# Kernel optimization log

Hardware: AMD Instinct MI355X
Metric: run time of the kernel (lower is better)

The kernel has to match this reference:

```python
import jax, jax.numpy as jnp
import numpy as np
from jax import lax

N, CI, CO, H, W = 2, 256, 256, 64, 64
K, G, DIL, PAD, STRIDE = 3, 8, 1, 1, 1
P = K * K
CG = CO // G  # group channels = 32


def setup_inputs() -> dict:
    key = jax.random.key(0)
    ks = jax.random.split(key, 24)
    r = lambda i, shape, s=1.0: jax.random.normal(ks[i], shape, jnp.float32) * s
    u = lambda i, shape: jax.random.uniform(ks[i], shape, jnp.float32, 0.5, 1.5)
    return dict(
        x=r(0, (N, CI, H, W)),
        conv1_w=r(1, (CO, CI), CI ** -0.5),
        bn1_g=u(2, (CO,)), bn1_b=r(3, (CO,), 0.1), bn1_m=r(4, (CO,), 0.1), bn1_v=u(5, (CO,)),
        inproj_w=r(6, (CO, CO), CO ** -0.5), inproj_b=r(7, (CO,), 0.02),
        dw_w=r(8, (CO, 1, K, K), 0.2), dw_b=r(9, (CO,), 0.02),
        ln_g=u(10, (CO,)), ln_b=r(11, (CO,), 0.02),
        off_w=r(12, (CO, G * P * 2), CO ** -0.5), off_b=jnp.zeros((G * P * 2,), jnp.float32),
        mask_w=r(13, (CO, G * P), CO ** -0.5), mask_b=jnp.zeros((G * P,), jnp.float32),
        outproj_w=r(14, (CO, CO), CO ** -0.5), outproj_b=r(15, (CO,), 0.02),
        bn2_g=u(16, (CO,)), bn2_b=r(17, (CO,), 0.1), bn2_m=r(18, (CO,), 0.1), bn2_v=u(19, (CO,)),
    )


def _bn(x, g, b, m, v, eps):
    # inference-mode BatchNorm2d on NCHW
    return (x - m[:, None, None]) * (g[:, None, None] * lax.rsqrt(v[:, None, None] + eps)) + b[:, None, None]


def _dcn_core(t, offset, mask):
    # t: (N,H,W,C) projected input; offset: (N,H,W,G*P*2); mask: (N,H,W,G,P) softmaxed
    xp = jnp.pad(t, ((0, 0), (PAD, PAD), (PAD, PAD), (0, 0)))
    H_, W_ = H + 2 * PAD, W + 2 * PAD
    # reference points (sample centers), normalized to padded size
    ry = ((DIL * (K - 1)) / 2 + 0.5 + STRIDE * jnp.arange(H, dtype=t.dtype)) / H_
    rx = ((DIL * (K - 1)) / 2 + 0.5 + STRIDE * jnp.arange(W, dtype=t.dtype)) / W_
    base = (DIL * (K - 1)) // 2
    gx = jnp.linspace(-base, -base + (K - 1) * DIL, K, dtype=t.dtype) / W_
    gy = jnp.linspace(-base, -base + (K - 1) * DIL, K, dtype=t.dtype) / H_
    gxx, gyy = jnp.meshgrid(gx, gy, indexing='ij')  # x varies along axis 0 (torch meshgrid order)
    grid = jnp.stack([gxx, gyy], -1).reshape(P, 2)  # (P,2)
    off = offset.reshape(N, H, W, G, P, 2) / jnp.array([W_, H_], t.dtype)
    loc_x = rx[None, None, :, None, None] + grid[:, 0][None, None, None, None] + off[..., 0]  # (N,H,W,G,P)
    loc_y = ry[None, :, None, None, None] + grid[:, 1][None, None, None, None] + off[..., 1]
    # grid_sample(align_corners=False): pixel = norm*size - 0.5
    px = jnp.transpose(loc_x * W_ - 0.5, (0, 3, 1, 2, 4)).reshape(N, G, H * W * P)
    py = jnp.transpose(loc_y * H_ - 0.5, (0, 3, 1, 2, 4)).reshape(N, G, H * W * P)
    # grouped channels-last image: (N,G,H_*W_,CG)
    xg = jnp.transpose(xp.reshape(N, H_, W_, G, CG), (0, 3, 1, 2, 4)).reshape(N, G, H_ * W_, CG)
    x0 = jnp.floor(px)
    y0 = jnp.floor(py)
    wx1 = px - x0
    wy1 = py - y0
    x0i = x0.astype(jnp.int32)
    y0i = y0.astype(jnp.int32)

    def corner(xi, yi, w):
        valid = (xi >= 0) & (xi <= W_ - 1) & (yi >= 0) & (yi <= H_ - 1)
        idx = jnp.clip(yi, 0, H_ - 1) * W_ + jnp.clip(xi, 0, W_ - 1)
        v = jnp.take_along_axis(xg, idx[..., None], axis=2)  # (N,G,M,CG)
        return v * jnp.where(valid, w, 0.0)[..., None]

    sampled = (corner(x0i, y0i, (1 - wx1) * (1 - wy1))
               + corner(x0i + 1, y0i, wx1 * (1 - wy1))
               + corner(x0i, y0i + 1, (1 - wx1) * wy1)
               + corner(x0i + 1, y0i + 1, wx1 * wy1))
    sampled = sampled.reshape(N, G, H * W, P, CG)
    mg = jnp.transpose(mask, (0, 3, 1, 2, 4)).reshape(N, G, H * W, P)
    out = jnp.einsum('nglpc,nglp->nglc', sampled, mg)
    return jnp.transpose(out, (0, 2, 1, 3)).reshape(N, H, W, G * CG)


def reference(x, conv1_w, bn1_g, bn1_b, bn1_m, bn1_v, inproj_w, inproj_b, dw_w, dw_b,
              ln_g, ln_b, off_w, off_b, mask_w, mask_b, outproj_w, outproj_b,
              bn2_g, bn2_b, bn2_m, bn2_v):
    # Conv(inc, ouc, k=1): 1x1 conv (no bias) + BN(eps=1e-3) + SiLU
    y = jnp.einsum('nchw,oc->nohw', x, conv1_w)
    y = jax.nn.silu(_bn(y, bn1_g, bn1_b, bn1_m, bn1_v, 1e-3))
    t = jnp.transpose(y, (0, 2, 3, 1))  # NHWC
    xproj = t @ inproj_w + inproj_b     # input_proj Linear
    # offset/mask branch: depthwise conv (k=3,s=1,p=1) -> LN over C -> GELU
    z = lax.conv_general_dilated(y, dw_w, (1, 1), ((PAD, PAD), (PAD, PAD)),
                                 feature_group_count=CO,
                                 dimension_numbers=('NCHW', 'OIHW', 'NCHW')) + dw_b[None, :, None, None]
    z = jnp.transpose(z, (0, 2, 3, 1))
    mu = jnp.mean(z, -1, keepdims=True)
    var = jnp.var(z, -1, keepdims=True)
    z = (z - mu) * lax.rsqrt(var + 1e-5) * ln_g + ln_b
    z = jax.nn.gelu(z, approximate=False)
    offset = z @ off_w + off_b  # (N,H,W,G*P*2)
    mask = jax.nn.softmax((z @ mask_w + mask_b).reshape(N, H, W, G, P), axis=-1)
    s = _dcn_core(xproj, offset, mask)
    s = s @ outproj_w + outproj_b  # output_proj Linear
    o = jnp.transpose(s, (0, 3, 1, 2))  # back to NCHW
    return jax.nn.silu(_bn(o, bn2_g, bn2_b, bn2_m, bn2_v, 1e-5))
```

## Files before the change

### kernel.cpp

```cpp
#include <hip/hip_runtime.h>
#include <hip/hip_fp16.h>
#include <math.h>

#define CC    256
#define HH    64
#define WW    64
#define HWSZ  4096
#define NPIX  8192
#define MT    32
#define TT    16
#define ASTR  264

typedef __attribute__((ext_vector_type(8))) _Float16 half8;
typedef __attribute__((ext_vector_type(4))) float f32x4;

__device__ __forceinline__ float silu_f(float x) { return x / (1.f + __expf(-x)); }

__device__ __forceinline__ short f2h(float f) {
    __half h = __float2half(f);
    return *reinterpret_cast<short*>(&h);
}
__device__ __forceinline__ unsigned h2u(float a, float b) {
    __half2 h = __floats2half2_rn(a, b);
    return *reinterpret_cast<unsigned*>(&h);
}
__device__ __forceinline__ __half2 u2h(unsigned v) { return *reinterpret_cast<__half2*>(&v); }
__device__ __forceinline__ unsigned h2raw(__half2 h) { return *reinterpret_cast<unsigned*>(&h); }
__device__ __forceinline__ float4 h2f4(uint2 u) {
    float2 a = __half22float2(u2h(u.x));
    float2 b = __half22float2(u2h(u.y));
    return make_float4(a.x, a.y, b.x, b.y);
}

__global__ __launch_bounds__(256) void k_prep(
        const float* __restrict__ cw, const float* __restrict__ ipw,
        const float* __restrict__ offw, const float* __restrict__ maskw,
        const float* __restrict__ opw, const float* __restrict__ dww,
        const float* __restrict__ offb, const float* __restrict__ maskb,
        const float* __restrict__ g1, const float* __restrict__ b1,
        const float* __restrict__ m1, const float* __restrict__ v1,
        const float* __restrict__ g2, const float* __restrict__ b2,
        const float* __restrict__ m2, const float* __restrict__ v2,
        short* __restrict__ Wc1b, short* __restrict__ Wipb,
        short* __restrict__ Whb, short* __restrict__ Wopb,
        float* __restrict__ dwt,
        float* __restrict__ bh, float* __restrict__ sc1, float* __restrict__ sh1,
        float* __restrict__ sc2, float* __restrict__ sh2) {
    __shared__ float tile[64 * 65];
    int t = threadIdx.x, bt = blockIdx.x;
    int ct = t & 63, rb = t >> 6;
    if (bt < 48) {
        int m = bt >> 4;
        int sub = bt & 15;
        int oT = (sub & 3) * 64, cT = (sub >> 2) * 64;
        const float* src = (m == 0) ? ipw : opw;
#pragma unroll
        for (int i = 0; i < 16; ++i) {
            int r = rb * 16 + i;
            int c = cT + r, o = oT + ct;
            float v;
            if (m < 2) v = src[c * CC + o];
            else v = (o < 144) ? offw[c * 144 + o]
                   : (o < 216) ? maskw[c * 72 + (o - 144)] : 0.f;
            tile[r * 65 + ct] = v;
        }
        __syncthreads();
        short* dst = (m == 0) ? Wipb : (m == 1) ? Wopb : Whb;
#pragma unroll
        for (int i = 0; i < 16; ++i) {
            int r = rb * 16 + i;
            dst[(size_t)(oT + r) * CC + cT + ct] = f2h(tile[ct * 65 + r]);
        }
    } else if (bt < 52) {
        int base = (bt - 48) * 16384;
#pragma unroll
        for (int i = 0; i < 16; ++i) {
            int idx = base + i * 1024 + t * 4;
            float4 v = *(const float4*)(cw + idx);
            *(uint2*)(Wc1b + idx) = make_uint2(h2u(v.x, v.y), h2u(v.z, v.w));
        }
    } else {
        int c = t;
#pragma unroll
        for (int j = 0; j < 9; ++j)
            dwt[j * CC + c] = dww[c * 9 + j];
        float bv = 0.f;
        if (c < 144) bv = offb[c];
        else if (c < 216) bv = maskb[c - 144];
        bh[c] = bv;
        float s1 = g1[c] * rsqrtf(v1[c] + 1e-3f);
        sc1[c] = s1; sh1[c] = b1[c] - m1[c] * s1;
        float s2 = g2[c] * rsqrtf(v2[c] + 1e-5f);
        sc2[c] = s2; sh2[c] = b2[c] - m2[c] * s2;
    }
}

__device__ __forceinline__ void gemm1(const short* As, const short* __restrict__ Wb,
                                      int lane, int n0, f32x4* acc) {
    const int m = lane & 15, q = lane >> 4;
#pragma unroll
    for (int kk = 0; kk < 8; ++kk) {
        int c0 = kk * 32 + q * 8;
        half8 a = *(const half8*)(As + m * ASTR + c0);
        half8 b = *(const half8*)(Wb + (size_t)(n0 + m) * CC + c0);
        *acc = __builtin_amdgcn_mfma_f32_16x16x32_f16(a, b, *acc, 0, 0, 0);
    }
}

__global__ __launch_bounds__(1024, 8) void k_conv_in(
        const float* __restrict__ x, const short* __restrict__ Wc1b,
        const short* __restrict__ Wipb, const float* __restrict__ sc1,
        const float* __restrict__ sh1, const float* __restrict__ ipb,
        short* __restrict__ ybf, short* __restrict__ xpb) {
    __shared__ __align__(16) short As[MT * ASTR];
    int tid = threadIdx.x, lane = tid & 63, wv = tid >> 6;
    int pix0 = blockIdx.x * MT;
    int n = pix0 >> 12, hw0 = pix0 & (HWSZ - 1);
    int n0 = wv * 16;
    const float* xn = x + (size_t)n * CC * HWSZ;
#pragma unroll
    for (int rep = 0; rep < 2; ++rep) {
        int f = tid + rep * 1024;
        int c = f >> 3, i8 = (f & 7) * 4;
        float4 v = *(const float4*)(xn + (size_t)c * HWSZ + hw0 + i8);
        As[(i8 + 0) * ASTR + c] = f2h(v.x);
        As[(i8 + 1) * ASTR + c] = f2h(v.y);
        As[(i8 + 2) * ASTR + c] = f2h(v.z);
        As[(i8 + 3) * ASTR + c] = f2h(v.w);
    }
    __syncthreads();
    f32x4 acc0 = (f32x4){0.f, 0.f, 0.f, 0.f};
    f32x4 acc1 = (f32x4){0.f, 0.f, 0.f, 0.f};
    gemm1(As, Wc1b, lane, n0, &acc0);
    gemm1(As + 16 * ASTR, Wc1b, lane, n0, &acc1);
    __syncthreads();
    int col = lane & 15, qr = (lane >> 4) * 4;
    int o = n0 + col;
    {
        float sc = sc1[o], sh = sh1[o];
#pragma unroll
        for (int r = 0; r < 4; ++r) {
            short v0 = f2h(silu_f(acc0[r] * sc + sh));
            As[(qr + r) * ASTR + o] = v0;
            ybf[(size_t)(pix0 + qr + r) * CC + o] = v0;
            short v1 = f2h(silu_f(acc1[r] * sc + sh));
            As[(16 + qr + r) * ASTR + o] = v1;
            ybf[(size_t)(pix0 + 16 + qr + r) * CC + o] = v1;
        }
    }
    __syncthreads();
    acc0 = (f32x4){0.f, 0.f, 0.f, 0.f};
    acc1 = (f32x4){0.f, 0.f, 0.f, 0.f};
    gemm1(As, Wipb, lane, n0, &acc0);
    gemm1(As + 16 * ASTR, Wipb, lane, n0, &acc1);
    {
        float bo = ipb[o];
#pragma unroll
        for (int r = 0; r < 4; ++r) {
            xpb[(size_t)(pix0 + qr + r) * CC + o] = f2h(acc0[r] + bo);
            xpb[(size_t)(pix0 + 16 + qr + r) * CC + o] = f2h(acc1[r] + bo);
        }
    }
}

__global__ __launch_bounds__(1024, 8) void k_tail(
        const short* __restrict__ ybf, const short* __restrict__ xpb,
        const float* __restrict__ dwt, const float* __restrict__ dwb,
        const float* __restrict__ lng, const float* __restrict__ lnb,
        const short* __restrict__ Whb, const float* __restrict__ bh,
        const short* __restrict__ Wopb, const float* __restrict__ opb,
        const float* __restrict__ sc2, const float* __restrict__ sh2,
        float* __restrict__ out) {
    __shared__ __align__(16) short As[TT * ASTR];
    __shared__ __align__(16) float buf[TT * 260];
    float* ml   = buf;
    float* loff = buf + 1536;
    float* xs   = buf;

    int tid = threadIdx.x, lane = tid & 63, wv = tid >> 6;
    int bid = blockIdx.x;
    int swz = ((bid & 7) << 6) | (bid >> 3);
    int pix0 = swz * TT;
    int n = pix0 >> 12, hw0 = pix0 & (HWSZ - 1);
    int h = hw0 >> 6, w0 = hw0 & 63;
    int c0 = lane * 4;
    int n0 = wv * 16;
    int col = lane & 15, qr = (lane >> 4) * 4;

    {
        float4 dwbv = *(const float4*)(dwb + c0);
        float4 lngv = *(const float4*)(lng + c0);
        float4 lnbv = *(const float4*)(lnb + c0);
        const short* yn = ybf + (size_t)n * HWSZ * CC;
        int pix = wv;
        int w = w0 + pix;
        float4 acc = dwbv;
        bool inter = (h > 0) && (h < HH - 1) && (w0 > 0) && (w0 < WW - TT);
        if (inter) {
#pragma unroll
            for (int ky = 0; ky < 3; ++ky) {
#pragma unroll
                for (int kx = 0; kx < 3; ++kx) {
                    int t = ky * 3 + kx;
                    float4 wt = *(const float4*)(dwt + t * CC + c0);
                    int idx = ((h + ky - 1) << 6) + (w + kx - 1);
                    float4 yv = h2f4(*(const uint2*)(yn + (size_t)idx * CC + c0));
                    acc.x += yv.x * wt.x;
                    acc.y += yv.y * wt.y;
                    acc.z += yv.z * wt.z;
                    acc.w += yv.w * wt.w;
                }
            }
        } else {
#pragma unroll
            for (int ky = 0; ky < 3; ++ky) {
                int yy = h + ky - 1;
                int yc = min(max(yy, 0), HH - 1);
                float vy = (yy == yc) ? 1.f : 0.f;
#pragma unroll
                for (int kx = 0; kx < 3; ++kx) {
                    int xx = w + kx - 1;
                    int xc = min(max(xx, 0), WW - 1);
                    float vm = vy * ((xx == xc) ? 1.f : 0.f);
                    int t = ky * 3 + kx;
                    float4 wt = *(const float4*)(dwt + t * CC + c0);
                    float4 yv = h2f4(*(const uint2*)(yn + (size_t)((yc << 6) + xc) * CC + c0));
                    acc.x += yv.x * wt.x * vm;
                    acc.y += yv.y * wt.y * vm;
                    acc.z += yv.z * wt.z * vm;
                    acc.w += yv.w * wt.w * vm;
                }
            }
        }
        float s1 = acc.x + acc.y + acc.z + acc.w;
        float s2 = acc.x * acc.x + acc.y * acc.y + acc.z * acc.z + acc.w * acc.w;
#pragma unroll
        for (int off = 32; off > 0; off >>= 1) {
            s1 += __shfl_xor(s1, off);
            s2 += __shfl_xor(s2, off);
        }
        float mu = s1 * (1.f / 256.f);
        float var = s2 * (1.f / 256.f) - mu * mu;
        float rs = rsqrtf(var + 1e-5f);
        float4 zv;
        zv.x = (acc.x - mu) * rs * lngv.x + lnbv.x;
        zv.y = (acc.y - mu) * rs * lngv.y + lnbv.y;
        zv.z = (acc.z - mu) * rs * lngv.z + lnbv.z;
        zv.w = (acc.w - mu) * rs * lngv.w + lnbv.w;
        zv.x = 0.5f * zv.x * (1.f + erff(zv.x * 0.70710678118654752f));
        zv.y = 0.5f * zv.y * (1.f + erff(zv.y * 0.70710678118654752f));
        zv.z = 0.5f * zv.z * (1.f + erff(zv.z * 0.70710678118654752f));
        zv.w = 0.5f * zv.w * (1.f + erff(zv.w * 0.70710678118654752f));
        *(uint2*)(As + pix * ASTR + c0) = make_uint2(h2u(zv.x, zv.y), h2u(zv.z, zv.w));
    }
    __syncthreads();

    {
        f32x4 acc = (f32x4){0.f, 0.f, 0.f, 0.f};
        gemm1(As, Whb, lane, n0, &acc);
        int o = n0 + col;
        float bo = bh[o];
#pragma unroll
        for (int r = 0; r < 4; ++r) {
            float v = acc[r] + bo;
            int pix = qr + r;
            if (o < 144) loff[pix * 144 + o] = v;
            else if (o < 216) {
                int mo = o - 144;
                int mg = (mo * 7282) >> 16;
                ml[pix * 96 + mg * 12 + (mo - mg * 9)] = v;
            }
        }
    }
    __syncthreads();

    {
        int g   = lane >> 3;
        int ci  = lane & 7;
        int cq  = ci & 3;
        int par = ci >> 2;
        int gc0 = g * 32 + cq * 8;
        int pix = wv;
        int w = w0 + pix;
        const float* row = ml + pix * 96 + g * 12;
        float4 r0 = *(const float4*)(row);
        float4 r1 = *(const float4*)(row + 4);
        float e0 = __expf(r0.x), e1 = __expf(r0.y), e2 = __expf(r0.z);
        float e3 = __expf(r0.w), e4 = __expf(r1.x), e5 = __expf(r1.y);
        float e6 = __expf(r1.z), e7 = __expf(r1.w), e8 = __expf(row[8]);
        float inv = 1.f / (e0 + e1 + e2 + e3 + e4 + e5 + e6 + e7 + e8);
        float m0 = (par ? e5 : e0) * inv;
        float m1 = (par ? e6 : e1) * inv;
        float m2 = (par ? e7 : e2) * inv;
        float m3 = (par ? e8 : e3) * inv;
        float m4 = e4 * inv;
        const float* lp = loff + pix * 144 + g * 18 + par * 10;
        const short* xpn = xpb + (size_t)n * HWSZ * CC;
        __half2 a0 = u2h(0u), a1 = u2h(0u), a2 = u2h(0u), a3 = u2h(0u);

        auto tapw = [&](float ox, float oy, int tx, int ty, float mval,
                        int& i00, int& i10, int& i01, int& i11,
                        float& w00, float& w10, float& w01, float& w11) {
            float px = (float)(w + tx) + ox;
            float py = (float)(h + ty) + oy;
            float fx = floorf(px), fy = floorf(py);
            float wx1 = px - fx, wy1 = py - fy;
            int x0 = (int)fx, y0 = (int)fy;
            int x1 = x0 + 1, y1 = y0 + 1;
            int xc0 = min(max(x0, 1), WW), xc1 = min(max(x1, 1), WW);
            int yc0 = min(max(y0, 1), HH), yc1 = min(max(y1, 1), HH);
            float vx0 = (x0 == xc0) ? 1.f : 0.f, vx1 = (x1 == xc1) ? 1.f : 0.f;
            float vy0 = (y0 == yc0) ? 1.f : 0.f, vy1 = (y1 == yc1) ? 1.f : 0.f;
            w00 = (1.f - wx1) * (1.f - wy1) * mval * vx0 * vy0;
            w10 = wx1 * (1.f - wy1) * mval * vx1 * vy0;
            w01 = (1.f - wx1) * wy1 * mval * vx0 * vy1;
            w11 = wx1 * wy1 * mval * vx1 * vy1;
            i00 = (((yc0 - 1) << 6) + (xc0 - 1)) * CC + gc0;
            i10 = (((yc0 - 1) << 6) + (xc1 - 1)) * CC + gc0;
            i01 = (((yc1 - 1) << 6) + (xc0 - 1)) * CC + gc0;
            i11 = (((yc1 - 1) << 6) + (xc1 - 1)) * CC + gc0;
        };
        auto fma4 = [&](uint4 u, float wgt) {
            __half2 W = __float2half2_rn(wgt);
            a0 = __hfma2(u2h(u.x), W, a0);
            a1 = __hfma2(u2h(u.y), W, a1);
            a2 = __hfma2(u2h(u.z), W, a2);
            a3 = __hfma2(u2h(u.w), W, a3);
        };

        int A00, A10, A01, A11, B00, B10, B01, B11;
        float Wa0, Wa1, Wa2, Wa3, Wb0, Wb1, Wb2, Wb3;
        float2 ofa = *(const float2*)(lp + 0);
        float2 ofb = *(const float2*)(lp + 2);
        tapw(ofa.x, ofa.y, par ? 1 : 0, par ? 2 : 0, m0, A00, A10, A01, A11, Wa0, Wa1, Wa2, Wa3);
        tapw(ofb.x, ofb.y, par ? 2 : 0, par ? 0 : 1, m1, B00, B10, B01, B11, Wb0, Wb1, Wb2, Wb3);
        {
            uint4 uA0 = *(const uint4*)(xpn + A00);
            uint4 uA1 = *(const uint4*)(xpn + A10);
            uint4 uA2 = *(const uint4*)(xpn + A01);
            uint4 uA3 = *(const uint4*)(xpn + A11);
            uint4 uB0 = *(const uint4*)(xpn + B00);
            uint4 uB1 = *(const uint4*)(xpn + B10);
            uint4 uB2 = *(const uint4*)(xpn + B01);
            uint4 uB3 = *(const uint4*)(xpn + B11);
            fma4(uA0, Wa0); fma4(uA1, Wa1); fma4(uA2, Wa2); fma4(uA3, Wa3);
            fma4(uB0, Wb0); fma4(uB1, Wb1); fma4(uB2, Wb2); fma4(uB3, Wb3);
        }
        ofa = *(const float2*)(lp + 4);
        ofb = *(const float2*)(lp + 6);
        tapw(ofa.x, ofa.y, par ? 2 : 0, par ? 1 : 2, m2, A00, A10, A01, A11, Wa0, Wa1, Wa2, Wa3);
        tapw(ofb.x, ofb.y, par ? 2 : 1, par ? 2 : 0, m3, B00, B10, B01, B11, Wb0, Wb1, Wb2, Wb3);
        {
            uint4 uA0 = *(const uint4*)(xpn + A00);
            uint4 uA1 = *(const uint4*)(xpn + A10);
            uint4 uA2 = *(const uint4*)(xpn + A01);
            uint4 uA3 = *(const uint4*)(xpn + A11);
            uint4 uB0 = *(const uint4*)(xpn + B00);
            uint4 uB1 = *(const uint4*)(xpn + B10);
            uint4 uB2 = *(const uint4*)(xpn + B01);
            uint4 uB3 = *(const uint4*)(xpn + B11);
            fma4(uA0, Wa0); fma4(uA1, Wa1); fma4(uA2, Wa2); fma4(uA3, Wa3);
            fma4(uB0, Wb0); fma4(uB1, Wb1); fma4(uB2, Wb2); fma4(uB3, Wb3);
        }
        if (!par) {
            ofa = *(const float2*)(lp + 8);
            tapw(ofa.x, ofa.y, 1, 1, m4, A00, A10, A01, A11, Wa0, Wa1, Wa2, Wa3);
            uint4 uA0 = *(const uint4*)(xpn + A00);
            uint4 uA1 = *(const uint4*)(xpn + A10);
            uint4 uA2 = *(const uint4*)(xpn + A01);
            uint4 uA3 = *(const uint4*)(xpn + A11);
            fma4(uA0, Wa0); fma4(uA1, Wa1); fma4(uA2, Wa2); fma4(uA3, Wa3);
        }
        a0 = __hadd2(a0, u2h((unsigned)__shfl_xor((int)h2raw(a0), 4)));
        a1 = __hadd2(a1, u2h((unsigned)__shfl_xor((int)h2raw(a1), 4)));
        a2 = __hadd2(a2, u2h((unsigned)__shfl_xor((int)h2raw(a2), 4)));
        a3 = __hadd2(a3, u2h((unsigned)__shfl_xor((int)h2raw(a3), 4)));
        if (!par)
            *(uint4*)(As + pix * ASTR + gc0) =
                make_uint4(h2raw(a0), h2raw(a1), h2raw(a2), h2raw(a3));
    }
    __syncthreads();

    {
        f32x4 acc = (f32x4){0.f, 0.f, 0.f, 0.f};
        gemm1(As, Wopb, lane, n0, &acc);
        int o = n0 + col;
        float bo = opb[o], sc = sc2[o], sh = sh2[o];
#pragma unroll
        for (int r = 0; r < 4; ++r)
            xs[(qr + r) * 260 + o] = silu_f((acc[r] + bo) * sc + sh);
    }
    __syncthreads();

    {
        int i4 = (tid & 3) * 4;
        int o = tid >> 2;
        float* on = out + (size_t)n * CC * HWSZ + hw0 + i4;
        float4 ov;
        ov.x = xs[(i4 + 0) * 260 + o];
        ov.y = xs[(i4 + 1) * 260 + o];
        ov.z = xs[(i4 + 2) * 260 + o];
        ov.w = xs[(i4 + 3) * 260 + o];
        *(float4*)(on + (size_t)o * HWSZ) = ov;
    }
}

extern "C" void kernel_launch(void* const* d_in, const int* in_sizes, int n_in,
                              void* d_out, int out_size, void* d_ws, size_t ws_size,
                              hipStream_t stream) {
    const float* x        = (const float*)d_in[0];
    const float* conv1_w  = (const float*)d_in[1];
    const float* bn1_g    = (const float*)d_in[2];
    const float* bn1_b    = (const float*)d_in[3];
    const float* bn1_m    = (const float*)d_in[4];
    const float* bn1_v    = (const float*)d_in[5];
    const float* inproj_w = (const float*)d_in[6];
    const float* inproj_b = (const float*)d_in[7];
    const float* dw_w     = (const float*)d_in[8];
    const float* dw_b     = (const float*)d_in[9];
    const float* ln_g     = (const float*)d_in[10];
    const float* ln_b     = (const float*)d_in[11];
    const float* off_w    = (const float*)d_in[12];
    const float* off_b    = (const float*)d_in[13];
    const float* mask_w   = (const float*)d_in[14];
    const float* mask_b   = (const float*)d_in[15];
    const float* outproj_w = (const float*)d_in[16];
    const float* outproj_b = (const float*)d_in[17];
    const float* bn2_g    = (const float*)d_in[18];
    const float* bn2_b    = (const float*)d_in[19];
    const float* bn2_m    = (const float*)d_in[20];
    const float* bn2_v    = (const float*)d_in[21];
    float* out = (float*)d_out;

    short* Wc1b = (short*)d_ws;
    short* Wipb = Wc1b + 65536;
    short* Whb  = Wipb + 65536;
    short* Wopb = Whb + 65536;
    float* fp   = (float*)(Wopb + 65536);
    float* dwt  = fp;
    float* bh   = dwt + 9 * CC;
    float* sc1  = bh + 256;
    float* sh1  = sc1 + 256;
    float* sc2  = sh1 + 256;
    float* sh2  = sc2 + 256;
    short* ybf  = (short*)(sh2 + 256);
    short* xpb  = ybf + (size_t)NPIX * CC;

    k_prep<<<dim3(53), dim3(256), 0, stream>>>(conv1_w, inproj_w, off_w, mask_w, outproj_w, dw_w,
                                               off_b, mask_b, bn1_g, bn1_b, bn1_m, bn1_v,
                                               bn2_g, bn2_b, bn2_m, bn2_v,
                                               Wc1b, Wipb, Whb, Wopb, dwt, bh, sc1, sh1, sc2, sh2);
    k_conv_in<<<dim3(NPIX / MT), dim3(1024), 0, stream>>>(x, Wc1b, Wipb, sc1, sh1, inproj_b, ybf, xpb);
    k_tail<<<dim3(NPIX / TT), dim3(1024), 0, stream>>>(ybf, xpb, dwt, dw_b, ln_g, ln_b,
                                                       Whb, bh, Wopb, outproj_b, sc2, sh2, out);
}
```

Baseline: 153.0 us.

## Fuse prep, input conv and tail into one persistent kernel with grid barriers

Merges the three kernels (weight prep, conv1+inproj, dwconv/offset/DCN/outproj tail) into a single launch of 512 blocks of 512 threads, separated by software grid barriers built on atomic counters. Each wave now computes two 16-column MFMA tiles instead of one, and tile sizes are unified to 16 pixels. Global writes of ybf/xpb are staged through LDS for coalesced stores. This removes launch gaps and inter-kernel drain. In exchange it adds a memset and spin barriers, and it requires all 512 blocks to be co-resident, which is a deadlock risk if occupancy is insufficient.

```diff
diff --git a/kernel.cpp b/kernel.cpp
--- a/kernel.cpp
+++ b/kernel.cpp
@@ -7,9 +7,9 @@
 #define WW    64
 #define HWSZ  4096
 #define NPIX  8192
-#define MT    32
 #define TT    16
 #define ASTR  264
+#define NBLK  512
 
 typedef __attribute__((ext_vector_type(8))) _Float16 half8;
 typedef __attribute__((ext_vector_type(4))) float f32x4;
@@ -32,255 +32,270 @@
     return make_float4(a.x, a.y, b.x, b.y);
 }
 
-__global__ __launch_bounds__(256) void k_prep(
-        const float* __restrict__ cw, const float* __restrict__ ipw,
-        const float* __restrict__ offw, const float* __restrict__ maskw,
-        const float* __restrict__ opw, const float* __restrict__ dww,
-        const float* __restrict__ offb, const float* __restrict__ maskb,
-        const float* __restrict__ g1, const float* __restrict__ b1,
-        const float* __restrict__ m1, const float* __restrict__ v1,
-        const float* __restrict__ g2, const float* __restrict__ b2,
-        const float* __restrict__ m2, const float* __restrict__ v2,
-        short* __restrict__ Wc1b, short* __restrict__ Wipb,
-        short* __restrict__ Whb, short* __restrict__ Wopb,
-        float* __restrict__ dwt,
-        float* __restrict__ bh, float* __restrict__ sc1, float* __restrict__ sh1,
-        float* __restrict__ sc2, float* __restrict__ sh2) {
-    __shared__ float tile[64 * 65];
-    int t = threadIdx.x, bt = blockIdx.x;
-    int ct = t & 63, rb = t >> 6;
-    if (bt < 48) {
-        int m = bt >> 4;
-        int sub = bt & 15;
+struct KParams {
+    const float *x, *cw, *ipw, *offw, *maskw, *opw, *dww;
+    const float *ipb, *dwb, *offb, *maskb, *lng, *lnb, *opb;
+    const float *g1, *b1, *m1, *v1, *g2, *b2, *m2, *v2;
+    short *Wc1b, *Wipb, *Whb, *Wopb;
+    float *dwt, *bh, *sc1, *sh1, *sc2, *sh2;
+    short *ybf, *xpb;
+    unsigned *bar0, *bar1;
+    float *out;
+};
+
+__device__ __forceinline__ void gridbar(unsigned* cnt) {
+    __syncthreads();
+    if (threadIdx.x == 0) {
+        __threadfence_system();
+        atomicAdd(cnt, 1u);
+        while (atomicAdd(cnt, 0u) < NBLK) __builtin_amdgcn_s_sleep(2);
+        __threadfence_system();
+    }
+    __syncthreads();
+}
+
+__device__ __forceinline__ void gemm2(const short* As, const short* __restrict__ Wb,
+                                      int lane, int n0, f32x4 acc[2]) {
+    const int m = lane & 15, q = lane >> 4;
+#pragma unroll
+    for (int kk = 0; kk < 8; ++kk) {
+        int c0 = kk * 32 + q * 8;
+        half8 a = *(const half8*)(As + m * ASTR + c0);
+#pragma unroll
+        for (int nt = 0; nt < 2; ++nt) {
+            half8 b = *(const half8*)(Wb + (size_t)(n0 + nt * 16 + m) * CC + c0);
+            acc[nt] = __builtin_amdgcn_mfma_f32_16x16x32_f16(a, b, acc[nt], 0, 0, 0);
+        }
+    }
+}
+
+__global__ __launch_bounds__(512, 4) void k_fused(KParams p) {
+    __shared__ __align__(16) short As[TT * ASTR];
+    __shared__ __align__(16) float buf[TT * 260];
+
+    int tid = threadIdx.x, lane = tid & 63, wv = tid >> 6;
+    int bid = blockIdx.x;
+
+    if (bid < 48) {
+        float* tile = buf;
+        int m = bid >> 4;
+        int sub = bid & 15;
         int oT = (sub & 3) * 64, cT = (sub >> 2) * 64;
-        const float* src = (m == 0) ? ipw : opw;
-#pragma unroll
-        for (int i = 0; i < 16; ++i) {
-            int r = rb * 16 + i;
+        int ct = tid & 63, rb = tid >> 6;
+        const float* src = (m == 0) ? p.ipw : p.opw;
+#pragma unroll
+        for (int i = 0; i < 8; ++i) {
+            int r = rb * 8 + i;
             int c = cT + r, o = oT + ct;
             float v;
             if (m < 2) v = src[c * CC + o];
-            else v = (o < 144) ? offw[c * 144 + o]
-                   : (o < 216) ? maskw[c * 72 + (o - 144)] : 0.f;
+            else v = (o < 144) ? p.offw[c * 144 + o]
+                   : (o < 216) ? p.maskw[c * 72 + (o - 144)] : 0.f;
             tile[r * 65 + ct] = v;
         }
         __syncthreads();
-        short* dst = (m == 0) ? Wipb : (m == 1) ? Wopb : Whb;
-#pragma unroll
-        for (int i = 0; i < 16; ++i) {
-            int r = rb * 16 + i;
+        short* dst = (m == 0) ? p.Wipb : (m == 1) ? p.Wopb : p.Whb;
+#pragma unroll
+        for (int i = 0; i < 8; ++i) {
+            int r = rb * 8 + i;
             dst[(size_t)(oT + r) * CC + cT + ct] = f2h(tile[ct * 65 + r]);
         }
-    } else if (bt < 52) {
-        int base = (bt - 48) * 16384;
-#pragma unroll
-        for (int i = 0; i < 16; ++i) {
-            int idx = base + i * 1024 + t * 4;
-            float4 v = *(const float4*)(cw + idx);
-            *(uint2*)(Wc1b + idx) = make_uint2(h2u(v.x, v.y), h2u(v.z, v.w));
-        }
-    } else {
-        int c = t;
+    } else if (bid < 52) {
+        int base = (bid - 48) * 16384;
+#pragma unroll
+        for (int i = 0; i < 8; ++i) {
+            int idx = base + i * 2048 + tid * 4;
+            float4 v = *(const float4*)(p.cw + idx);
+            *(uint2*)(p.Wc1b + idx) = make_uint2(h2u(v.x, v.y), h2u(v.z, v.w));
+        }
+    } else if (bid == 52 && tid < 256) {
+        int c = tid;
 #pragma unroll
         for (int j = 0; j < 9; ++j)
-            dwt[j * CC + c] = dww[c * 9 + j];
+            p.dwt[j * CC + c] = p.dww[c * 9 + j];
         float bv = 0.f;
-        if (c < 144) bv = offb[c];
-        else if (c < 216) bv = maskb[c - 144];
-        bh[c] = bv;
-        float s1 = g1[c] * rsqrtf(v1[c] + 1e-3f);
-        sc1[c] = s1; sh1[c] = b1[c] - m1[c] * s1;
-        float s2 = g2[c] * rsqrtf(v2[c] + 1e-5f);
-        sc2[c] = s2; sh2[c] = b2[c] - m2[c] * s2;
-    }
-}
-
-__device__ __forceinline__ void gemm1(const short* As, const short* __restrict__ Wb,
-                                      int lane, int n0, f32x4* acc) {
-    const int m = lane & 15, q = lane >> 4;
-#pragma unroll
-    for (int kk = 0; kk < 8; ++kk) {
-        int c0 = kk * 32 + q * 8;
-        half8 a = *(const half8*)(As + m * ASTR + c0);
-        half8 b = *(const half8*)(Wb + (size_t)(n0 + m) * CC + c0);
-        *acc = __builtin_amdgcn_mfma_f32_16x16x32_f16(a, b, *acc, 0, 0, 0);
-    }
-}
-
-__global__ __launch_bounds__(1024, 8) void k_conv_in(
-        const float* __restrict__ x, const short* __restrict__ Wc1b,
-        const short* __restrict__ Wipb, const float* __restrict__ sc1,
-        const float* __restrict__ sh1, const float* __restrict__ ipb,
-        short* __restrict__ ybf, short* __restrict__ xpb) {
-    __shared__ __align__(16) short As[MT * ASTR];
-    int tid = threadIdx.x, lane = tid & 63, wv = tid >> 6;
-    int pix0 = blockIdx.x * MT;
-    int n = pix0 >> 12, hw0 = pix0 & (HWSZ - 1);
-    int n0 = wv * 16;
-    const float* xn = x + (size_t)n * CC * HWSZ;
-#pragma unroll
-    for (int rep = 0; rep < 2; ++rep) {
-        int f = tid + rep * 1024;
-        int c = f >> 3, i8 = (f & 7) * 4;
-        float4 v = *(const float4*)(xn + (size_t)c * HWSZ + hw0 + i8);
-        As[(i8 + 0) * ASTR + c] = f2h(v.x);
-        As[(i8 + 1) * ASTR + c] = f2h(v.y);
-        As[(i8 + 2) * ASTR + c] = f2h(v.z);
-        As[(i8 + 3) * ASTR + c] = f2h(v.w);
-    }
-    __syncthreads();
-    f32x4 acc0 = (f32x4){0.f, 0.f, 0.f, 0.f};
-    f32x4 acc1 = (f32x4){0.f, 0.f, 0.f, 0.f};
-    gemm1(As, Wc1b, lane, n0, &acc0);
-    gemm1(As + 16 * ASTR, Wc1b, lane, n0, &acc1);
-    __syncthreads();
-    int col = lane & 15, qr = (lane >> 4) * 4;
-    int o = n0 + col;
-    {
-        float sc = sc1[o], sh = sh1[o];
-#pragma unroll
-        for (int r = 0; r < 4; ++r) {
-            short v0 = f2h(silu_f(acc0[r] * sc + sh));
-            As[(qr + r) * ASTR + o] = v0;
-            ybf[(size_t)(pix0 + qr + r) * CC + o] = v0;
-            short v1 = f2h(silu_f(acc1[r] * sc + sh));
-            As[(16 + qr + r) * ASTR + o] = v1;
-            ybf[(size_t)(pix0 + 16 + qr + r) * CC + o] = v1;
-        }
-    }
-    __syncthreads();
-    acc0 = (f32x4){0.f, 0.f, 0.f, 0.f};
-    acc1 = (f32x4){0.f, 0.f, 0.f, 0.f};
-    gemm1(As, Wipb, lane, n0, &acc0);
-    gemm1(As + 16 * ASTR, Wipb, lane, n0, &acc1);
-    {
-        float bo = ipb[o];
-#pragma unroll
-        for (int r = 0; r < 4; ++r) {
-            xpb[(size_t)(pix0 + qr + r) * CC + o] = f2h(acc0[r] + bo);
-            xpb[(size_t)(pix0 + 16 + qr + r) * CC + o] = f2h(acc1[r] + bo);
-        }
-    }
-}
-
-__global__ __launch_bounds__(1024, 8) void k_tail(
-        const short* __restrict__ ybf, const short* __restrict__ xpb,
-        const float* __restrict__ dwt, const float* __restrict__ dwb,
-        const float* __restrict__ lng, const float* __restrict__ lnb,
-        const short* __restrict__ Whb, const float* __restrict__ bh,
-        const short* __restrict__ Wopb, const float* __restrict__ opb,
-        const float* __restrict__ sc2, const float* __restrict__ sh2,
-        float* __restrict__ out) {
-    __shared__ __align__(16) short As[TT * ASTR];
-    __shared__ __align__(16) float buf[TT * 260];
+        if (c < 144) bv = p.offb[c];
+        else if (c < 216) bv = p.maskb[c - 144];
+        p.bh[c] = bv;
+        float s1 = p.g1[c] * rsqrtf(p.v1[c] + 1e-3f);
+        p.sc1[c] = s1; p.sh1[c] = p.b1[c] - p.m1[c] * s1;
+        float s2 = p.g2[c] * rsqrtf(p.v2[c] + 1e-5f);
+        p.sc2[c] = s2; p.sh2[c] = p.b2[c] - p.m2[c] * s2;
+    }
+    gridbar(p.bar0);
+
+    {
+        int pix0 = bid * TT;
+        int n = pix0 >> 12, hw0 = pix0 & (HWSZ - 1);
+        int n0 = wv * 32;
+        const float* xn = p.x + (size_t)n * CC * HWSZ;
+#pragma unroll
+        for (int rep = 0; rep < 2; ++rep) {
+            int f = tid + rep * 512;
+            int c = f >> 2, i4 = (f & 3) * 4;
+            float4 v = *(const float4*)(xn + (size_t)c * HWSZ + hw0 + i4);
+            As[(i4 + 0) * ASTR + c] = f2h(v.x);
+            As[(i4 + 1) * ASTR + c] = f2h(v.y);
+            As[(i4 + 2) * ASTR + c] = f2h(v.z);
+            As[(i4 + 3) * ASTR + c] = f2h(v.w);
+        }
+        __syncthreads();
+        f32x4 acc[2];
+        acc[0] = (f32x4){0.f, 0.f, 0.f, 0.f};
+        acc[1] = (f32x4){0.f, 0.f, 0.f, 0.f};
+        gemm2(As, p.Wc1b, lane, n0, acc);
+        __syncthreads();
+        int col = lane & 15, qr = (lane >> 4) * 4;
+#pragma unroll
+        for (int nt = 0; nt < 2; ++nt) {
+            int o = n0 + nt * 16 + col;
+            float sc = p.sc1[o], sh = p.sh1[o];
+#pragma unroll
+            for (int r = 0; r < 4; ++r)
+                As[(qr + r) * ASTR + o] = f2h(silu_f(acc[nt][r] * sc + sh));
+        }
+        __syncthreads();
+#pragma unroll
+        for (int rr = 0; rr < 2; ++rr) {
+            int row = wv * 2 + rr;
+            *(uint2*)(p.ybf + (size_t)(pix0 + row) * CC + lane * 4) =
+                *(const uint2*)(As + row * ASTR + lane * 4);
+        }
+        acc[0] = (f32x4){0.f, 0.f, 0.f, 0.f};
+        acc[1] = (f32x4){0.f, 0.f, 0.f, 0.f};
+        gemm2(As, p.Wipb, lane, n0, acc);
+        __syncthreads();
+#pragma unroll
+        for (int nt = 0; nt < 2; ++nt) {
+            int o = n0 + nt * 16 + col;
+            float bo = p.ipb[o];
+#pragma unroll
+            for (int r = 0; r < 4; ++r)
+                As[(qr + r) * ASTR + o] = f2h(acc[nt][r] + bo);
+        }
+        __syncthreads();
+#pragma unroll
+        for (int rr = 0; rr < 2; ++rr) {
+            int row = wv * 2 + rr;
+            *(uint2*)(p.xpb + (size_t)(pix0 + row) * CC + lane * 4) =
+                *(const uint2*)(As + row * ASTR + lane * 4);
+        }
+    }
+    gridbar(p.bar1);
+
     float* ml   = buf;
     float* loff = buf + 1536;
     float* xs   = buf;
 
-    int tid = threadIdx.x, lane = tid & 63, wv = tid >> 6;
-    int bid = blockIdx.x;
     int swz = ((bid & 7) << 6) | (bid >> 3);
     int pix0 = swz * TT;
     int n = pix0 >> 12, hw0 = pix0 & (HWSZ - 1);
     int h = hw0 >> 6, w0 = hw0 & 63;
     int c0 = lane * 4;
-    int n0 = wv * 16;
+    int n0 = wv * 32;
     int col = lane & 15, qr = (lane >> 4) * 4;
 
     {
-        float4 dwbv = *(const float4*)(dwb + c0);
-        float4 lngv = *(const float4*)(lng + c0);
-        float4 lnbv = *(const float4*)(lnb + c0);
-        const short* yn = ybf + (size_t)n * HWSZ * CC;
-        int pix = wv;
-        int w = w0 + pix;
-        float4 acc = dwbv;
+        float4 dwbv = *(const float4*)(p.dwb + c0);
+        float4 lngv = *(const float4*)(p.lng + c0);
+        float4 lnbv = *(const float4*)(p.lnb + c0);
+        const short* yn = p.ybf + (size_t)n * HWSZ * CC;
         bool inter = (h > 0) && (h < HH - 1) && (w0 > 0) && (w0 < WW - TT);
-        if (inter) {
-#pragma unroll
-            for (int ky = 0; ky < 3; ++ky) {
-#pragma unroll
-                for (int kx = 0; kx < 3; ++kx) {
-                    int t = ky * 3 + kx;
-                    float4 wt = *(const float4*)(dwt + t * CC + c0);
-                    int idx = ((h + ky - 1) << 6) + (w + kx - 1);
-                    float4 yv = h2f4(*(const uint2*)(yn + (size_t)idx * CC + c0));
-                    acc.x += yv.x * wt.x;
-                    acc.y += yv.y * wt.y;
-                    acc.z += yv.z * wt.z;
-                    acc.w += yv.w * wt.w;
+#pragma unroll
+        for (int i = 0; i < 2; ++i) {
+            int pix = wv * 2 + i;
+            int w = w0 + pix;
+            float4 acc = dwbv;
+            if (inter) {
+#pragma unroll
+                for (int ky = 0; ky < 3; ++ky) {
+#pragma unroll
+                    for (int kx = 0; kx < 3; ++kx) {
+                        int t = ky * 3 + kx;
+                        float4 wt = *(const float4*)(p.dwt + t * CC + c0);
+                        int idx = ((h + ky - 1) << 6) + (w + kx - 1);
+                        float4 yv = h2f4(*(const uint2*)(yn + (size_t)idx * CC + c0));
+                        acc.x += yv.x * wt.x;
+                        acc.y += yv.y * wt.y;
+                        acc.z += yv.z * wt.z;
+                        acc.w += yv.w * wt.w;
+                    }
+                }
+            } else {
+#pragma unroll
+                for (int ky = 0; ky < 3; ++ky) {
+                    int yy = h + ky - 1;
+                    int yc = min(max(yy, 0), HH - 1);
+                    float vy = (yy == yc) ? 1.f : 0.f;
+#pragma unroll
+                    for (int kx = 0; kx < 3; ++kx) {
+                        int xx = w + kx - 1;
+                        int xc = min(max(xx, 0), WW - 1);
+                        float vm = vy * ((xx == xc) ? 1.f : 0.f);
+                        int t = ky * 3 + kx;
+                        float4 wt = *(const float4*)(p.dwt + t * CC + c0);
+                        float4 yv = h2f4(*(const uint2*)(yn + (size_t)((yc << 6) + xc) * CC + c0));
+                        acc.x += yv.x * wt.x * vm;
+                        acc.y += yv.y * wt.y * vm;
+                        acc.z += yv.z * wt.z * vm;
+                        acc.w += yv.w * wt.w * vm;
+                    }
                 }
             }
-        } else {
-#pragma unroll
-            for (int ky = 0; ky < 3; ++ky) {
-                int yy = h + ky - 1;
-                int yc = min(max(yy, 0), HH - 1);
-                float vy = (yy == yc) ? 1.f : 0.f;
-#pragma unroll
-                for (int kx = 0; kx < 3; ++kx) {
-                    int xx = w + kx - 1;
-                    int xc = min(max(xx, 0), WW - 1);
-                    float vm = vy * ((xx == xc) ? 1.f : 0.f);
-                    int t = ky * 3 + kx;
-                    float4 wt = *(const float4*)(dwt + t * CC + c0);
-                    float4 yv = h2f4(*(const uint2*)(yn + (size_t)((yc << 6) + xc) * CC + c0));
-                    acc.x += yv.x * wt.x * vm;
-                    acc.y += yv.y * wt.y * vm;
-                    acc.z += yv.z * wt.z * vm;
-                    acc.w += yv.w * wt.w * vm;
+            float s1 = acc.x + acc.y + acc.z + acc.w;
+            float s2 = acc.x * acc.x + acc.y * acc.y + acc.z * acc.z + acc.w * acc.w;
+#pragma unroll
+            for (int off = 32; off > 0; off >>= 1) {
+                s1 += __shfl_xor(s1, off);
+                s2 += __shfl_xor(s2, off);
+            }
+            float mu = s1 * (1.f / 256.f);
+            float var = s2 * (1.f / 256.f) - mu * mu;
+            float rs = rsqrtf(var + 1e-5f);
+            float4 zv;
+            zv.x = (acc.x - mu) * rs * lngv.x + lnbv.x;
+            zv.y = (acc.y - mu) * rs * lngv.y + lnbv.y;
+            zv.z = (acc.z - mu) * rs * lngv.z + lnbv.z;
+            zv.w = (acc.w - mu) * rs * lngv.w + lnbv.w;
+            zv.x = 0.5f * zv.x * (1.f + erff(zv.x * 0.70710678118654752f));
+            zv.y = 0.5f * zv.y * (1.f + erff(zv.y * 0.70710678118654752f));
+            zv.z = 0.5f * zv.z * (1.f + erff(zv.z * 0.70710678118654752f));
+            zv.w = 0.5f * zv.w * (1.f + erff(zv.w * 0.70710678118654752f));
+            *(uint2*)(As + pix * ASTR + c0) = make_uint2(h2u(zv.x, zv.y), h2u(zv.z, zv.w));
+        }
+    }
+    __syncthreads();
+
+    {
+        f32x4 acc[2];
+        acc[0] = (f32x4){0.f, 0.f, 0.f, 0.f};
+        acc[1] = (f32x4){0.f, 0.f, 0.f, 0.f};
+        gemm2(As, p.Whb, lane, n0, acc);
+#pragma unroll
+        for (int nt = 0; nt < 2; ++nt) {
+            int o = n0 + nt * 16 + col;
+            float bo = p.bh[o];
+#pragma unroll
+            for (int r = 0; r < 4; ++r) {
+                float v = acc[nt][r] + bo;
+                int pix = qr + r;
+                if (o < 144) loff[pix * 144 + o] = v;
+                else if (o < 216) {
+                    int mo = o - 144;
+                    int mg = (mo * 7282) >> 16;
+                    ml[pix * 96 + mg * 12 + (mo - mg * 9)] = v;
                 }
             }
         }
-        float s1 = acc.x + acc.y + acc.z + acc.w;
-        float s2 = acc.x * acc.x + acc.y * acc.y + acc.z * acc.z + acc.w * acc.w;
-#pragma unroll
-        for (int off = 32; off > 0; off >>= 1) {
-            s1 += __shfl_xor(s1, off);
-            s2 += __shfl_xor(s2, off);
-        }
-        float mu = s1 * (1.f / 256.f);
-        float var = s2 * (1.f / 256.f) - mu * mu;
-        float rs = rsqrtf(var + 1e-5f);
-        float4 zv;
-        zv.x = (acc.x - mu) * rs * lngv.x + lnbv.x;
-        zv.y = (acc.y - mu) * rs * lngv.y + lnbv.y;
-        zv.z = (acc.z - mu) * rs * lngv.z + lnbv.z;
-        zv.w = (acc.w - mu) * rs * lngv.w + lnbv.w;
-        zv.x = 0.5f * zv.x * (1.f + erff(zv.x * 0.70710678118654752f));
-        zv.y = 0.5f * zv.y * (1.f + erff(zv.y * 0.70710678118654752f));
-        zv.z = 0.5f * zv.z * (1.f + erff(zv.z * 0.70710678118654752f));
-        zv.w = 0.5f * zv.w * (1.f + erff(zv.w * 0.70710678118654752f));
-        *(uint2*)(As + pix * ASTR + c0) = make_uint2(h2u(zv.x, zv.y), h2u(zv.z, zv.w));
-    }
-    __syncthreads();
-
-    {
-        f32x4 acc = (f32x4){0.f, 0.f, 0.f, 0.f};
-        gemm1(As, Whb, lane, n0, &acc);
-        int o = n0 + col;
-        float bo = bh[o];
-#pragma unroll
-        for (int r = 0; r < 4; ++r) {
-            float v = acc[r] + bo;
-            int pix = qr + r;
-            if (o < 144) loff[pix * 144 + o] = v;
-            else if (o < 216) {
-                int mo = o - 144;
-                int mg = (mo * 7282) >> 16;
-                ml[pix * 96 + mg * 12 + (mo - mg * 9)] = v;
-            }
-        }
-    }
-    __syncthreads();
-
-    {
-        int g   = lane >> 3;
-        int ci  = lane & 7;
-        int cq  = ci & 3;
-        int par = ci >> 2;
+    }
+    __syncthreads();
+
+    {
+        int ph = lane >> 5;
+        int g  = (lane >> 2) & 7;
+        int cq = lane & 3;
         int gc0 = g * 32 + cq * 8;
-        int pix = wv;
+        int pix = wv * 2 + ph;
         int w = w0 + pix;
         const float* row = ml + pix * 96 + g * 12;
         float4 r0 = *(const float4*)(row);
@@ -289,13 +304,11 @@
         float e3 = __expf(r0.w), e4 = __expf(r1.x), e5 = __expf(r1.y);
         float e6 = __expf(r1.z), e7 = __expf(r1.w), e8 = __expf(row[8]);
         float inv = 1.f / (e0 + e1 + e2 + e3 + e4 + e5 + e6 + e7 + e8);
-        float m0 = (par ? e5 : e0) * inv;
-        float m1 = (par ? e6 : e1) * inv;
-        float m2 = (par ? e7 : e2) * inv;
-        float m3 = (par ? e8 : e3) * inv;
-        float m4 = e4 * inv;
-        const float* lp = loff + pix * 144 + g * 18 + par * 10;
-        const short* xpn = xpb + (size_t)n * HWSZ * CC;
+        float m0 = e0 * inv, m1 = e1 * inv, m2 = e2 * inv;
+        float m3 = e3 * inv, m4 = e4 * inv, m5 = e5 * inv;
+        float m6 = e6 * inv, m7 = e7 * inv, m8 = e8 * inv;
+        const float* lp = loff + pix * 144 + g * 18;
+        const short* xpn = p.xpb + (size_t)n * HWSZ * CC;
         __half2 a0 = u2h(0u), a1 = u2h(0u), a2 = u2h(0u), a3 = u2h(0u);
 
         auto tapw = [&](float ox, float oy, int tx, int ty, float mval,
@@ -327,14 +340,12 @@
             a2 = __hfma2(u2h(u.z), W, a2);
             a3 = __hfma2(u2h(u.w), W, a3);
         };
-
-        int A00, A10, A01, A11, B00, B10, B01, B11;
-        float Wa0, Wa1, Wa2, Wa3, Wb0, Wb1, Wb2, Wb3;
-        float2 ofa = *(const float2*)(lp + 0);
-        float2 ofb = *(const float2*)(lp + 2);
-        tapw(ofa.x, ofa.y, par ? 1 : 0, par ? 2 : 0, m0, A00, A10, A01, A11, Wa0, Wa1, Wa2, Wa3);
-        tapw(ofb.x, ofb.y, par ? 2 : 0, par ? 0 : 1, m1, B00, B10, B01, B11, Wb0, Wb1, Wb2, Wb3);
-        {
+        auto pair = [&](float2 ofa, float2 ofb, int txa, int tya, int txb, int tyb,
+                        float ma, float mb) {
+            int A00, A10, A01, A11, B00, B10, B01, B11;
+            float Wa0, Wa1, Wa2, Wa3, Wb0, Wb1, Wb2, Wb3;
+            tapw(ofa.x, ofa.y, txa, tya, ma, A00, A10, A01, A11, Wa0, Wa1, Wa2, Wa3);
+            tapw(ofb.x, ofb.y, txb, tyb, mb, B00, B10, B01, B11, Wb0, Wb1, Wb2, Wb3);
             uint4 uA0 = *(const uint4*)(xpn + A00);
             uint4 uA1 = *(const uint4*)(xpn + A10);
             uint4 uA2 = *(const uint4*)(xpn + A01);
@@ -345,93 +356,63 @@
             uint4 uB3 = *(const uint4*)(xpn + B11);
             fma4(uA0, Wa0); fma4(uA1, Wa1); fma4(uA2, Wa2); fma4(uA3, Wa3);
             fma4(uB0, Wb0); fma4(uB1, Wb1); fma4(uB2, Wb2); fma4(uB3, Wb3);
-        }
-        ofa = *(const float2*)(lp + 4);
-        ofb = *(const float2*)(lp + 6);
-        tapw(ofa.x, ofa.y, par ? 2 : 0, par ? 1 : 2, m2, A00, A10, A01, A11, Wa0, Wa1, Wa2, Wa3);
-        tapw(ofb.x, ofb.y, par ? 2 : 1, par ? 2 : 0, m3, B00, B10, B01, B11, Wb0, Wb1, Wb2, Wb3);
+        };
+        pair(*(const float2*)(lp + 0),  *(const float2*)(lp + 2),  0, 0, 0, 1, m0, m1);
+        pair(*(const float2*)(lp + 4),  *(const float2*)(lp + 6),  0, 2, 1, 0, m2, m3);
+        pair(*(const float2*)(lp + 8),  *(const float2*)(lp + 10), 1, 1, 1, 2, m4, m5);
+        pair(*(const float2*)(lp + 12), *(const float2*)(lp + 14), 2, 0, 2, 1, m6, m7);
         {
-            uint4 uA0 = *(const uint4*)(xpn + A00);
-            uint4 uA1 = *(const uint4*)(xpn + A10);
-            uint4 uA2 = *(const uint4*)(xpn + A01);
-            uint4 uA3 = *(const uint4*)(xpn + A11);
-            uint4 uB0 = *(const uint4*)(xpn + B00);
-            uint4 uB1 = *(const uint4*)(xpn + B10);
-            uint4 uB2 = *(const uint4*)(xpn + B01);
-            uint4 uB3 = *(const uint4*)(xpn + B11);
-            fma4(uA0, Wa0); fma4(uA1, Wa1); fma4(uA2, Wa2); fma4(uA3, Wa3);
-            fma4(uB0, Wb0); fma4(uB1, Wb1); fma4(uB2, Wb2); fma4(uB3, Wb3);
-        }
-        if (!par) {
-            ofa = *(const float2*)(lp + 8);
-            tapw(ofa.x, ofa.y, 1, 1, m4, A00, A10, A01, A11, Wa0, Wa1, Wa2, Wa3);
+            float2 ofa = *(const float2*)(lp + 16);
+            int A00, A10, A01, A11;
+            float Wa0, Wa1, Wa2, Wa3;
+            tapw(ofa.x, ofa.y, 2, 2, m8, A00, A10, A01, A11, Wa0, Wa1, Wa2, Wa3);
             uint4 uA0 = *(const uint4*)(xpn + A00);
             uint4 uA1 = *(const uint4*)(xpn + A10);
             uint4 uA2 = *(const uint4*)(xpn + A01);
             uint4 uA3 = *(const uint4*)(xpn + A11);
             fma4(uA0, Wa0); fma4(uA1, Wa1); fma4(uA2, Wa2); fma4(uA3, Wa3);
         }
-        a0 = __hadd2(a0, u2h((unsigned)__shfl_xor((int)h2raw(a0), 4)));
-        a1 = __hadd2(a1, u2h((unsigned)__shfl_xor((int)h2raw(a1), 4)));
-        a2 = __hadd2(a2, u2h((unsigned)__shfl_xor((int)h2raw(a2), 4)));
-        a3 = __hadd2(a3, u2h((unsigned)__shfl_xor((int)h2raw(a3), 4)));
-        if (!par)
-            *(uint4*)(As + pix * ASTR + gc0) =
-                make_uint4(h2raw(a0), h2raw(a1), h2raw(a2), h2raw(a3));
-    }
-    __syncthreads();
-
-    {
-        f32x4 acc = (f32x4){0.f, 0.f, 0.f, 0.f};
-        gemm1(As, Wopb, lane, n0, &acc);
-        int o = n0 + col;
-        float bo = opb[o], sc = sc2[o], sh = sh2[o];
-#pragma unroll
-        for (int r = 0; r < 4; ++r)
-            xs[(qr + r) * 260 + o] = silu_f((acc[r] + bo) * sc + sh);
+        *(uint4*)(As + pix * ASTR + gc0) =
+            make_uint4(h2raw(a0), h2raw(a1), h2raw(a2), h2raw(a3));
+    }
+    __syncthreads();
+
+    {
+        f32x4 acc[2];
+        acc[0] = (f32x4){0.f, 0.f, 0.f, 0.f};
+        acc[1] = (f32x4){0.f, 0.f, 0.f, 0.f};
+        gemm2(As, p.Wopb, lane, n0, acc);
+#pragma unroll
+        for (int nt = 0; nt < 2; ++nt) {
+            int o = n0 + nt * 16 + col;
+            float bo = p.opb[o], sc = p.sc2[o], sh = p.sh2[o];
+#pragma unroll
+            for (int r = 0; r < 4; ++r)
+                xs[(qr + r) * 260 + o] = silu_f((acc[nt][r] + bo) * sc + sh);
+        }
     }
     __syncthreads();
 
     {
         int i4 = (tid & 3) * 4;
-        int o = tid >> 2;
-        float* on = out + (size_t)n * CC * HWSZ + hw0 + i4;
-        float4 ov;
-        ov.x = xs[(i4 + 0) * 260 + o];
-        ov.y = xs[(i4 + 1) * 260 + o];
-        ov.z = xs[(i4 + 2) * 260 + o];
-        ov.w = xs[(i4 + 3) * 260 + o];
-        *(float4*)(on + (size_t)o * HWSZ) = ov;
+        int obase = tid >> 2;
+        float* on = p.out + (size_t)n * CC * HWSZ + hw0 + i4;
+#pragma unroll
+        for (int pass = 0; pass < 2; ++pass) {
+            int o = obase + pass * 128;
+            float4 ov;
+            ov.x = xs[(i4 + 0) * 260 + o];
+            ov.y = xs[(i4 + 1) * 260 + o];
+            ov.z = xs[(i4 + 2) * 260 + o];
+            ov.w = xs[(i4 + 3) * 260 + o];
+            *(float4*)(on + (size_t)o * HWSZ) = ov;
+        }
     }
 }
 
 extern "C" void kernel_launch(void* const* d_in, const int* in_sizes, int n_in,
                               void* d_out, int out_size, void* d_ws, size_t ws_size,
                               hipStream_t stream) {
-    const float* x        = (const float*)d_in[0];
-    const float* conv1_w  = (const float*)d_in[1];
-    const float* bn1_g    = (const float*)d_in[2];
-    const float* bn1_b    = (const float*)d_in[3];
-    const float* bn1_m    = (const float*)d_in[4];
-    const float* bn1_v    = (const float*)d_in[5];
-    const float* inproj_w = (const float*)d_in[6];
-    const float* inproj_b = (const float*)d_in[7];
-    const float* dw_w     = (const float*)d_in[8];
-    const float* dw_b     = (const float*)d_in[9];
-    const float* ln_g     = (const float*)d_in[10];
-    const float* ln_b     = (const float*)d_in[11];
-    const float* off_w    = (const float*)d_in[12];
-    const float* off_b    = (const float*)d_in[13];
-    const float* mask_w   = (const float*)d_in[14];
-    const float* mask_b   = (const float*)d_in[15];
-    const float* outproj_w = (const float*)d_in[16];
-    const float* outproj_b = (const float*)d_in[17];
-    const float* bn2_g    = (const float*)d_in[18];
-    const float* bn2_b    = (const float*)d_in[19];
-    const float* bn2_m    = (const float*)d_in[20];
-    const float* bn2_v    = (const float*)d_in[21];
-    float* out = (float*)d_out;
-
     short* Wc1b = (short*)d_ws;
     short* Wipb = Wc1b + 65536;
     short* Whb  = Wipb + 65536;
@@ -445,12 +426,37 @@
     float* sh2  = sc2 + 256;
     short* ybf  = (short*)(sh2 + 256);
     short* xpb  = ybf + (size_t)NPIX * CC;
-
-    k_prep<<<dim3(53), dim3(256), 0, stream>>>(conv1_w, inproj_w, off_w, mask_w, outproj_w, dw_w,
-                                               off_b, mask_b, bn1_g, bn1_b, bn1_m, bn1_v,
-                                               bn2_g, bn2_b, bn2_m, bn2_v,
-                                               Wc1b, Wipb, Whb, Wopb, dwt, bh, sc1, sh1, sc2, sh2);
-    k_conv_in<<<dim3(NPIX / MT), dim3(1024), 0, stream>>>(x, Wc1b, Wipb, sc1, sh1, inproj_b, ybf, xpb);
-    k_tail<<<dim3(NPIX / TT), dim3(1024), 0, stream>>>(ybf, xpb, dwt, dw_b, ln_g, ln_b,
-                                                       Whb, bh, Wopb, outproj_b, sc2, sh2, out);
-}
+    unsigned* bar = (unsigned*)(xpb + (size_t)NPIX * CC);
+
+    KParams p;
+    p.x     = (const float*)d_in[0];
+    p.cw    = (const float*)d_in[1];
+    p.g1    = (const float*)d_in[2];
+    p.b1    = (const float*)d_in[3];
+    p.m1    = (const float*)d_in[4];
+    p.v1    = (const float*)d_in[5];
+    p.ipw   = (const float*)d_in[6];
+    p.ipb   = (const float*)d_in[7];
+    p.dww   = (const float*)d_in[8];
+    p.dwb   = (const float*)d_in[9];
+    p.lng   = (const float*)d_in[10];
+    p.lnb   = (const float*)d_in[11];
+    p.offw  = (const float*)d_in[12];
+    p.offb  = (const float*)d_in[13];
+    p.maskw = (const float*)d_in[14];
+    p.maskb = (const float*)d_in[15];
+    p.opw   = (const float*)d_in[16];
+    p.opb   = (const float*)d_in[17];
+    p.g2    = (const float*)d_in[18];
+    p.b2    = (const float*)d_in[19];
+    p.m2    = (const float*)d_in[20];
+    p.v2    = (const float*)d_in[21];
+    p.Wc1b = Wc1b; p.Wipb = Wipb; p.Whb = Whb; p.Wopb = Wopb;
+    p.dwt = dwt; p.bh = bh; p.sc1 = sc1; p.sh1 = sh1; p.sc2 = sc2; p.sh2 = sh2;
+    p.ybf = ybf; p.xpb = xpb;
+    p.bar0 = bar; p.bar1 = bar + 1;
+    p.out = (float*)d_out;
+
+    hipMemsetAsync(bar, 0, 2 * sizeof(unsigned), stream);
+    k_fused<<<dim3(NBLK), dim3(512), 0, stream>>>(p);
+}
```

Result: slower. 232.2 us (+51.8%).
